# Optimization experiments

Measured on AMD Instinct MI355X. Metric: run time of the kernel, lower is better.

Reference implementation:

```python
import jax, jax.numpy as jnp
import numpy as np

N = 8192
D_IN = 60
NUM_CLASSES = 10


def _xavier(key, out_f, in_f):
    limit = float(np.sqrt(6.0 / (in_f + out_f)))
    return jax.random.uniform(key, (out_f, in_f), jnp.float32, -limit, limit)


def setup_inputs() -> dict:
    key = jax.random.key(0)
    ks = jax.random.split(key, 10)
    return {
        "x": jax.random.normal(ks[0], (N, D_IN), jnp.float32),
        "fc1_w": _xavier(ks[1], 32, 60),
        "fc1_b": jnp.zeros((32,), jnp.float32),
        "fc2_w": _xavier(ks[2], 16, 32),
        "fc2_b": jnp.zeros((16,), jnp.float32),
        "fc3_w": _xavier(ks[3], 8, 60),
        "fc3_b": jnp.zeros((8,), jnp.float32),
        "fc6_w": _xavier(ks[4], NUM_CLASSES, 8),
        "fc6_b": jnp.zeros((NUM_CLASSES,), jnp.float32),
        "temp": jnp.float32(1.0) + 0.1 * jax.random.truncated_normal(ks[5], -2.0, 2.0, (), jnp.float32),
        "theta": jnp.float32(1.0) + 0.1 * jax.random.truncated_normal(ks[6], -2.0, 2.0, (), jnp.float32),
    }


def _pairwise_sq_dist(z):
    # z: [N, d] -> [N, N] squared euclidean distances, clamped at 0
    sq = jnp.sum(z * z, axis=1)  # [N]
    dist = sq[:, None] + sq[None, :] - 2.0 * (z @ z.T)
    return jnp.maximum(dist, 0.0)


def reference(x, fc1_w, fc1_b, fc2_w, fc2_b, fc3_w, fc3_b, fc6_w, fc6_b, temp, theta):
    net = x @ fc1_w.T + fc1_b           # [N, 32]
    net = net @ fc2_w.T + fc2_b         # [N, 16]
    A = -_pairwise_sq_dist(net)         # [N, N]
    A = jax.nn.sigmoid(temp * A + theta)
    # A * (1 - I) + I == set diagonal to 1
    A = jnp.fill_diagonal(A, 1.0, inplace=False)
    A = A / jnp.sum(A, axis=1, keepdims=True)
    h = A @ x                           # [N, 60] dense graph aggregation
    h = h @ fc3_w.T + fc3_b             # [N, 8]
    return jax.nn.softmax(h @ fc6_w.T + fc6_b, axis=1)  # [N, num_classes]
```

## Files before the change

### kernel.cpp

```cpp
#include <hip/hip_runtime.h>
#include <math.h>

#define NROWS 8192
#define DIN   60
#define DZ    16
#define NC    10

#define LOG2E 1.4426950408889634f

#define RB  256
#define CJ  512
#define NRB (NROWS / RB)
#define NCH (NROWS / CJ)

typedef short bf16x8 __attribute__((ext_vector_type(8)));
typedef float f32x4  __attribute__((ext_vector_type(4)));

__device__ __forceinline__ unsigned int bfr(float f) {
    return (__float_as_uint(f) + 0x8000u) >> 16;
}

__global__ __launch_bounds__(256) void k1_embed(
    const float* __restrict__ x,
    const float* __restrict__ w1, const float* __restrict__ b1,
    const float* __restrict__ w2, const float* __restrict__ b2,
    const float* __restrict__ temp_p, const float* __restrict__ theta_p,
    unsigned short* __restrict__ zb, float* __restrict__ bbf)
{
    int i = blockIdx.x * 256 + threadIdx.x;

    float xr[DIN];
    const float4* xp = reinterpret_cast<const float4*>(x + (size_t)i * DIN);
    #pragma unroll
    for (int c = 0; c < 15; ++c) {
        float4 v = xp[c];
        xr[c*4+0] = v.x; xr[c*4+1] = v.y; xr[c*4+2] = v.z; xr[c*4+3] = v.w;
    }

    float n1[32];
    #pragma unroll
    for (int o = 0; o < 32; ++o) {
        float acc = b1[o];
        #pragma unroll
        for (int k = 0; k < DIN; ++k) acc = fmaf(w1[o*DIN+k], xr[k], acc);
        n1[o] = acc;
    }

    float z[DZ];
    float sq = 0.0f;
    #pragma unroll
    for (int u = 0; u < DZ; ++u) {
        float acc = b2[u];
        #pragma unroll
        for (int o = 0; o < 32; ++o) acc = fmaf(w2[u*32+o], n1[o], acc);
        z[u] = acc;
        sq = fmaf(acc, acc, sq);
    }

    float temp  = *temp_p;
    float theta = *theta_p;
    float s = sqrtf(2.0f * temp * LOG2E);

    unsigned int p[8];
    #pragma unroll
    for (int u = 0; u < 8; ++u) {
        unsigned int lo = bfr(z[2*u]   * s);
        unsigned int hi = bfr(z[2*u+1] * s);
        p[u] = lo | (hi << 16);
    }
    uint4* dst = reinterpret_cast<uint4*>(zb + (size_t)i * 32);
    dst[0] = make_uint4(p[0], p[1], p[2], p[3]);
    dst[1] = make_uint4(p[4], p[5], p[6], p[7]);
    dst[2] = make_uint4(0, 0, 0, 0);
    dst[3] = make_uint4(0, 0, 0, 0);

    bbf[i] = LOG2E * fmaf(temp, sq, -0.5f * theta);
}

__global__ __launch_bounds__(256) void k1_xt(
    const float* __restrict__ x, unsigned short* __restrict__ xT)
{
    int i = blockIdx.x * 256 + threadIdx.x;
    float xr[DIN];
    const float4* xp = reinterpret_cast<const float4*>(x + (size_t)i * DIN);
    #pragma unroll
    for (int c = 0; c < 15; ++c) {
        float4 v = xp[c];
        xr[c*4+0] = v.x; xr[c*4+1] = v.y; xr[c*4+2] = v.z; xr[c*4+3] = v.w;
    }
    #pragma unroll
    for (int c = 0; c < DIN; ++c)
        xT[(size_t)c * NROWS + i] = (unsigned short)bfr(xr[c]);
    xT[(size_t)60 * NROWS + i] = 0x3F80;
    xT[(size_t)61 * NROWS + i] = 0;
    xT[(size_t)62 * NROWS + i] = 0;
    xT[(size_t)63 * NROWS + i] = 0;
}

__global__ __launch_bounds__(512, 4) void k2_mfma(
    const unsigned short* __restrict__ zb, const float* __restrict__ bbf,
    const unsigned short* __restrict__ xT, const float* __restrict__ theta_p,
    float* __restrict__ hacc)
{
    __shared__ unsigned long long sP[8 * 320];

    const int tid  = threadIdx.x;
    const int lane = tid & 63, wave = tid >> 6;
    const int q = lane & 15, g = lane >> 4;
    const int rb = blockIdx.x & (NRB - 1);
    const int ch = blockIdx.x / NRB;
    const int i0 = rb * RB + wave * 32;
    const int j0 = ch * CJ;

    bf16x8 zbi[2];
    float  bi[2];
    #pragma unroll
    for (int t = 0; t < 2; ++t) {
        zbi[t] = *reinterpret_cast<const bf16x8*>(zb + (size_t)(i0 + t*16 + q) * 32 + g*8);
        bi[t]  = bbf[i0 + t*16 + q];
    }
    const float nclamp = -(*theta_p) * LOG2E;
    const f32x4 z4 = {0.0f, 0.0f, 0.0f, 0.0f};

    f32x4 H[2][4];
    #pragma unroll
    for (int t = 0; t < 2; ++t)
        #pragma unroll
        for (int nt = 0; nt < 4; ++nt) H[t][nt] = z4;

    char* myP = reinterpret_cast<char*>(sP) + wave * 2560;

    for (int jp = 0; jp < CJ / 32; ++jp) {
        #pragma unroll
        for (int half = 0; half < 2; ++half) {
            const int gj = j0 + jp*32 + half*16;
            bf16x8 za = *reinterpret_cast<const bf16x8*>(zb + (size_t)(gj + q) * 32 + g*8);
            f32x4  bj = *reinterpret_cast<const f32x4*>(bbf + gj + 4*g);
            #pragma unroll
            for (int t = 0; t < 2; ++t) {
                f32x4 S = __builtin_amdgcn_mfma_f32_16x16x32_bf16(za, zbi[t], z4, 0, 0, 0);
                unsigned int ur[4];
                #pragma unroll
                for (int r = 0; r < 4; ++r) {
                    float n = (bi[t] + bj[r]) - S[r];
                    n = fmaxf(n, nclamp);
                    float P = __builtin_amdgcn_rcpf(1.0f + __builtin_amdgcn_exp2f(n));
                    if (i0 + t*16 == gj && q == 4*g + r) P = 0.0f;
                    ur[r] = __float_as_uint(P) + 0x8000u;
                }
                unsigned int pk0 = (ur[0] >> 16) | (ur[1] & 0xFFFF0000u);
                unsigned int pk1 = (ur[2] >> 16) | (ur[3] & 0xFFFF0000u);
                *reinterpret_cast<unsigned long long*>(
                    myP + t*1280 + q*80 + half*32 + g*8) =
                    ((unsigned long long)pk1 << 32) | pk0;
            }
        }
        const int jb = j0 + jp*32;
        bf16x8 pa[2];
        #pragma unroll
        for (int t = 0; t < 2; ++t)
            pa[t] = *reinterpret_cast<const bf16x8*>(myP + t*1280 + q*80 + g*16);
        #pragma unroll
        for (int nt = 0; nt < 4; ++nt) {
            bf16x8 xb = *reinterpret_cast<const bf16x8*>(
                xT + (size_t)(nt*16 + q) * NROWS + jb + g*8);
            H[0][nt] = __builtin_amdgcn_mfma_f32_16x16x32_bf16(pa[0], xb, H[0][nt], 0, 0, 0);
            H[1][nt] = __builtin_amdgcn_mfma_f32_16x16x32_bf16(pa[1], xb, H[1][nt], 0, 0, 0);
        }
    }

    #pragma unroll
    for (int t = 0; t < 2; ++t)
        #pragma unroll
        for (int nt = 0; nt < 4; ++nt)
            #pragma unroll
            for (int r = 0; r < 4; ++r) {
                int row = i0 + t*16 + 4*g + r;
                hacc[((size_t)ch * NROWS + row) * 64 + nt*16 + q] = H[t][nt][r];
            }
}

__global__ __launch_bounds__(256) void k3_reduce(float* __restrict__ hacc)
{
    const int tid = threadIdx.x;
    const int r   = blockIdx.x * 32 + (tid >> 3);
    const int c   = (tid & 7) * 8;

    float s[8];
    #pragma unroll
    for (int k = 0; k < 8; ++k) s[k] = 0.0f;

    for (int ch = 0; ch < NCH; ++ch) {
        const float4* p = reinterpret_cast<const float4*>(
            hacc + ((size_t)ch * NROWS + r) * 64 + c);
        float4 v0 = p[0], v1 = p[1];
        s[0] += v0.x; s[1] += v0.y; s[2] += v0.z; s[3] += v0.w;
        s[4] += v1.x; s[5] += v1.y; s[6] += v1.z; s[7] += v1.w;
    }

    float4* q = reinterpret_cast<float4*>(hacc + (size_t)r * 64 + c);
    q[0] = make_float4(s[0], s[1], s[2], s[3]);
    q[1] = make_float4(s[4], s[5], s[6], s[7]);
}

__global__ __launch_bounds__(256) void k3_head(
    const float* __restrict__ x,
    const float* __restrict__ w3, const float* __restrict__ b3,
    const float* __restrict__ w6, const float* __restrict__ b6,
    const float* __restrict__ hacc,
    float* __restrict__ out)
{
    int i = blockIdx.x * 256 + threadIdx.x;

    const float* hi = hacc + (size_t)i * 64;
    const float* xi = x + (size_t)i * DIN;

    float rd = __builtin_amdgcn_rcpf(hi[60] + 1.0f);

    float h[DIN];
    #pragma unroll
    for (int k = 0; k < DIN; ++k) h[k] = (hi[k] + xi[k]) * rd;

    float g[8];
    #pragma unroll
    for (int o = 0; o < 8; ++o) {
        float a = b3[o];
        #pragma unroll
        for (int k = 0; k < DIN; ++k) a = fmaf(w3[o*DIN+k], h[k], a);
        g[o] = a;
    }

    float l[NC];
    float m = -3.0e38f;
    #pragma unroll
    for (int c = 0; c < NC; ++c) {
        float a = b6[c];
        #pragma unroll
        for (int o = 0; o < 8; ++o) a = fmaf(w6[c*8+o], g[o], a);
        l[c] = a;
        m = fmaxf(m, a);
    }
    float e[NC];
    float sum = 0.0f;
    #pragma unroll
    for (int c = 0; c < NC; ++c) {
        e[c] = __builtin_amdgcn_exp2f((l[c] - m) * LOG2E);
        sum += e[c];
    }
    float rsum = __builtin_amdgcn_rcpf(sum);
    #pragma unroll
    for (int c = 0; c < NC; ++c) out[(size_t)i * NC + c] = e[c] * rsum;
}

extern "C" void kernel_launch(void* const* d_in, const int* in_sizes, int n_in,
                              void* d_out, int out_size, void* d_ws, size_t ws_size,
                              hipStream_t stream)
{
    const float* x     = (const float*)d_in[0];
    const float* w1    = (const float*)d_in[1];
    const float* b1    = (const float*)d_in[2];
    const float* w2    = (const float*)d_in[3];
    const float* b2    = (const float*)d_in[4];
    const float* w3    = (const float*)d_in[5];
    const float* b3    = (const float*)d_in[6];
    const float* w6    = (const float*)d_in[7];
    const float* b6    = (const float*)d_in[8];
    const float* temp  = (const float*)d_in[9];
    const float* theta = (const float*)d_in[10];
    float* out = (float*)d_out;

    char* p = (char*)d_ws;
    unsigned short* zbuf = (unsigned short*)p;  p += (size_t)NROWS * 32 * 2;
    float*          bbf  = (float*)p;           p += (size_t)NROWS * 4;
    unsigned short* xT   = (unsigned short*)p;  p += (size_t)64 * NROWS * 2;
    float*          hbuf = (float*)p;

    k1_embed<<<NROWS / 256, 256, 0, stream>>>(x, w1, b1, w2, b2, temp, theta, zbuf, bbf);
    k1_xt   <<<NROWS / 256, 256, 0, stream>>>(x, xT);
    k2_mfma <<<NRB * NCH, 512, 0, stream>>>(zbuf, bbf, xT, theta, hbuf);
    k3_reduce<<<NROWS / 32, 256, 0, stream>>>(hbuf);
    k3_head <<<NROWS / 256, 256, 0, stream>>>(x, w3, b3, w6, b6, hbuf, out);
}
```

Before: 181.0 us.

## Fuse embed and transpose kernels, halve column chunk, shrink blocks for more parallelism

Result: slower. 218.4 us (+20.7%).

```diff
diff --git a/kernel.cpp b/kernel.cpp
--- a/kernel.cpp
+++ b/kernel.cpp
@@ -9,7 +9,7 @@
 #define LOG2E 1.4426950408889634f
 
 #define RB  256
-#define CJ  512
+#define CJ  256
 #define NRB (NROWS / RB)
 #define NCH (NROWS / CJ)
 
@@ -20,14 +20,15 @@
     return (__float_as_uint(f) + 0x8000u) >> 16;
 }
 
-__global__ __launch_bounds__(256) void k1_embed(
+__global__ __launch_bounds__(64) void k1_all(
     const float* __restrict__ x,
     const float* __restrict__ w1, const float* __restrict__ b1,
     const float* __restrict__ w2, const float* __restrict__ b2,
     const float* __restrict__ temp_p, const float* __restrict__ theta_p,
-    unsigned short* __restrict__ zb, float* __restrict__ bbf)
-{
-    int i = blockIdx.x * 256 + threadIdx.x;
+    unsigned short* __restrict__ zb, float* __restrict__ bbf,
+    unsigned short* __restrict__ xT)
+{
+    int i = blockIdx.x * 64 + threadIdx.x;
 
     float xr[DIN];
     const float4* xp = reinterpret_cast<const float4*>(x + (size_t)i * DIN);
@@ -75,19 +76,7 @@
     dst[3] = make_uint4(0, 0, 0, 0);
 
     bbf[i] = LOG2E * fmaf(temp, sq, -0.5f * theta);
-}
-
-__global__ __launch_bounds__(256) void k1_xt(
-    const float* __restrict__ x, unsigned short* __restrict__ xT)
-{
-    int i = blockIdx.x * 256 + threadIdx.x;
-    float xr[DIN];
-    const float4* xp = reinterpret_cast<const float4*>(x + (size_t)i * DIN);
-    #pragma unroll
-    for (int c = 0; c < 15; ++c) {
-        float4 v = xp[c];
-        xr[c*4+0] = v.x; xr[c*4+1] = v.y; xr[c*4+2] = v.z; xr[c*4+3] = v.w;
-    }
+
     #pragma unroll
     for (int c = 0; c < DIN; ++c)
         xT[(size_t)c * NROWS + i] = (unsigned short)bfr(xr[c]);
@@ -97,7 +86,7 @@
     xT[(size_t)63 * NROWS + i] = 0;
 }
 
-__global__ __launch_bounds__(512, 4) void k2_mfma(
+__global__ __launch_bounds__(512, 8) void k2_mfma(
     const unsigned short* __restrict__ zb, const float* __restrict__ bbf,
     const unsigned short* __restrict__ xT, const float* __restrict__ theta_p,
     float* __restrict__ hacc)
@@ -108,7 +97,7 @@
     const int lane = tid & 63, wave = tid >> 6;
     const int q = lane & 15, g = lane >> 4;
     const int rb = blockIdx.x & (NRB - 1);
-    const int ch = blockIdx.x / NRB;
+    const int ch = blockIdx.x >> 5;
     const int i0 = rb * RB + wave * 32;
     const int j0 = ch * CJ;
 
@@ -183,34 +172,27 @@
 __global__ __launch_bounds__(256) void k3_reduce(float* __restrict__ hacc)
 {
     const int tid = threadIdx.x;
-    const int r   = blockIdx.x * 32 + (tid >> 3);
-    const int c   = (tid & 7) * 8;
-
-    float s[8];
-    #pragma unroll
-    for (int k = 0; k < 8; ++k) s[k] = 0.0f;
-
+    const int r   = blockIdx.x * 16 + (tid >> 4);
+    const int c   = (tid & 15) * 4;
+
+    float4 s = make_float4(0.0f, 0.0f, 0.0f, 0.0f);
+    #pragma unroll 4
     for (int ch = 0; ch < NCH; ++ch) {
-        const float4* p = reinterpret_cast<const float4*>(
+        float4 v = *reinterpret_cast<const float4*>(
             hacc + ((size_t)ch * NROWS + r) * 64 + c);
-        float4 v0 = p[0], v1 = p[1];
-        s[0] += v0.x; s[1] += v0.y; s[2] += v0.z; s[3] += v0.w;
-        s[4] += v1.x; s[5] += v1.y; s[6] += v1.z; s[7] += v1.w;
-    }
-
-    float4* q = reinterpret_cast<float4*>(hacc + (size_t)r * 64 + c);
-    q[0] = make_float4(s[0], s[1], s[2], s[3]);
-    q[1] = make_float4(s[4], s[5], s[6], s[7]);
-}
-
-__global__ __launch_bounds__(256) void k3_head(
+        s.x += v.x; s.y += v.y; s.z += v.z; s.w += v.w;
+    }
+    *reinterpret_cast<float4*>(hacc + (size_t)r * 64 + c) = s;
+}
+
+__global__ __launch_bounds__(64) void k3_head(
     const float* __restrict__ x,
     const float* __restrict__ w3, const float* __restrict__ b3,
     const float* __restrict__ w6, const float* __restrict__ b6,
     const float* __restrict__ hacc,
     float* __restrict__ out)
 {
-    int i = blockIdx.x * 256 + threadIdx.x;
+    int i = blockIdx.x * 64 + threadIdx.x;
 
     const float* hi = hacc + (size_t)i * 64;
     const float* xi = x + (size_t)i * DIN;
@@ -275,9 +257,8 @@
     unsigned short* xT   = (unsigned short*)p;  p += (size_t)64 * NROWS * 2;
     float*          hbuf = (float*)p;
 
-    k1_embed<<<NROWS / 256, 256, 0, stream>>>(x, w1, b1, w2, b2, temp, theta, zbuf, bbf);
-    k1_xt   <<<NROWS / 256, 256, 0, stream>>>(x, xT);
+    k1_all  <<<NROWS / 64, 64, 0, stream>>>(x, w1, b1, w2, b2, temp, theta, zbuf, bbf, xT);
     k2_mfma <<<NRB * NCH, 512, 0, stream>>>(zbuf, bbf, xT, theta, hbuf);
-    k3_reduce<<<NROWS / 32, 256, 0, stream>>>(hbuf);
-    k3_head <<<NROWS / 256, 256, 0, stream>>>(x, w3, b3, w6, b6, hbuf, out);
-}
+    k3_reduce<<<NROWS / 16, 256, 0, stream>>>(hbuf);
+    k3_head <<<NROWS / 64, 64, 0, stream>>>(x, w3, b3, w6, b6, hbuf, out);
+}
```
